# Kernel optimization log

Hardware: AMD Instinct MI355X
Metric: run time of the kernel (lower is better)

## Reference

```python
import jax, jax.numpy as jnp
import numpy as np

H = 4  # pairwise_num_attention_heads

def _layer_norm(x, gamma, beta, eps=1e-5):
    mu = jnp.mean(x, axis=-1, keepdims=True)
    var = jnp.var(x, axis=-1, keepdims=True)
    return (x - mu) * jax.lax.rsqrt(var + eps) * gamma + beta

def setup_inputs() -> dict:
    key = jax.random.key(0)
    ks = jax.random.split(key, 8)
    B, L, P = 1, 256, 128
    s = 0.02
    return {
        "pairwise_states": jax.random.normal(ks[0], (B, L, L, P), jnp.float32),
        "ln_gamma": jnp.ones((P,), jnp.float32),
        "ln_beta": jnp.zeros((P,), jnp.float32),
        "Wq": jax.random.normal(ks[1], (P, P), jnp.float32) * s,
        "Wk": jax.random.normal(ks[2], (P, P), jnp.float32) * s,
        "Wv": jax.random.normal(ks[3], (P, P), jnp.float32) * s,
        "Wb": jax.random.normal(ks[4], (P, H), jnp.float32) * s,
        "Wg": jax.random.normal(ks[5], (P, P), jnp.float32) * s,
        "bg": jnp.zeros((P,), jnp.float32),
        "Wo": jax.random.normal(ks[6], (P, P), jnp.float32) * s,
        "bo": jnp.zeros((P,), jnp.float32),
    }

def reference(pairwise_states, ln_gamma, ln_beta, Wq, Wk, Wv, Wb, Wg, bg, Wo, bo):
    # Row-axis triangle attention (RibonanzaNetPairwiseAttention, axis='row', eval mode).
    B, L, _, P = pairwise_states.shape
    D = P // H  # attention_head_size
    x = _layer_norm(pairwise_states, ln_gamma, ln_beta)  # [b,i,j,p]
    q = (x @ Wq).reshape(B, L, L, H, D)
    k = (x @ Wk).reshape(B, L, L, H, D)
    v = (x @ Wv).reshape(B, L, L, H, D)
    scale = jnp.asarray(D, x.dtype) ** 0.5
    # pairwise bias: [b,i,j,h] -> broadcast over the row axis of the scores
    bias = jnp.einsum('bijp,ph->bhij', x, Wb)  # [b,h,L,L]
    # scores[b,h,i,j,k]: within row i, query position j attends to key position k
    scores = jnp.einsum('bijhd,bikhd->bhijk', q, k) / scale + bias[:, :, None]
    probs = jax.nn.softmax(scores, axis=-1)
    ctx = jnp.einsum('bhijk,bikhd->bijhd', probs, v).reshape(B, L, L, P)
    gate = jax.nn.sigmoid(x @ Wg + bg)
    ctx = gate * ctx
    # output dense + residual (AxisDropout is identity in eval mode)
    return ctx @ Wo + bo + pairwise_states
```

## Files before the change

### kernel.cpp

```cpp
#include <hip/hip_runtime.h>

#define NPOS 65536

typedef __attribute__((ext_vector_type(8))) short bf16x8;
typedef __attribute__((ext_vector_type(4))) float f32x4;

#if __has_builtin(__builtin_amdgcn_exp2f)
#define EXP2F(x) __builtin_amdgcn_exp2f(x)
#else
#define EXP2F(x) __expf((x) * 0.6931471805599453f)
#endif
#if __has_builtin(__builtin_amdgcn_rcpf)
#define RCPF(x) __builtin_amdgcn_rcpf(x)
#else
#define RCPF(x) (1.0f / (x))
#endif

static __device__ __forceinline__ unsigned short f2bf(float f) {
  union { float f; unsigned int u; } v; v.f = f;
  unsigned int r = v.u + 0x7fffu + ((v.u >> 16) & 1u);
  return (unsigned short)(r >> 16);
}
static __device__ __forceinline__ float lo_bf(unsigned int u) {
  union { unsigned int u; float f; } v; v.u = u << 16; return v.f;
}
static __device__ __forceinline__ float hi_bf(unsigned int u) {
  union { unsigned int u; float f; } v; v.u = u & 0xffff0000u; return v.f;
}
static __device__ __forceinline__ unsigned int permpack(float hi, float lo) {
  union { float f; unsigned int u; } a, b;
  a.f = hi; b.f = lo;
#if __has_builtin(__builtin_amdgcn_perm)
  return __builtin_amdgcn_perm(a.u, b.u, 0x07060302u);
#else
  return (a.u & 0xffff0000u) | (b.u >> 16);
#endif
}

__global__ void k_pack(const float* __restrict__ Wq, const float* __restrict__ Wk,
                       const float* __restrict__ Wv, const float* __restrict__ Wg,
                       const float* __restrict__ Wo,
                       ushort* __restrict__ WT, ushort* __restrict__ WoT) {
  int idx = blockIdx.x * blockDim.x + threadIdx.x;
  if (idx < 512 * 128) {
    int n = idx >> 7, k = idx & 127;
    int nn = n & 127;
    float val;
    if (n < 128)      val = Wq[k * 128 + nn] * (0.17677669529663687f * 1.4426950408889634f);
    else if (n < 256) val = Wk[k * 128 + nn];
    else if (n < 384) val = Wv[k * 128 + nn];
    else              val = Wg[k * 128 + nn];
    WT[idx] = f2bf(val);
  } else if (idx < 512 * 128 + 128 * 128) {
    int j = idx - 512 * 128;
    int n = j >> 7, k = j & 127;
    WoT[j] = f2bf(Wo[k * 128 + n]);
  }
}

__global__ __launch_bounds__(128, 4) void k_lnbias(
    const float* __restrict__ in, const float* __restrict__ gamma,
    const float* __restrict__ beta, const float* __restrict__ Wb,
    ushort* __restrict__ biasB) {
  int t = threadIdx.x, wv = t >> 6, lane = t & 63;
  int n = lane & 15, g = lane >> 4;
  int myrow = blockIdx.x * 32 + wv * 16 + n;
  const float* rp = in + (size_t)myrow * 128;

  float xv[32];
  float sm = 0.f, ssm = 0.f;
  #pragma unroll
  for (int kc = 0; kc < 4; kc++)
    #pragma unroll
    for (int pr = 0; pr < 2; pr++) {
      float4 v = *(const float4*)(rp + kc * 32 + g * 8 + pr * 4);
      int o = kc * 8 + pr * 4;
      xv[o] = v.x; xv[o+1] = v.y; xv[o+2] = v.z; xv[o+3] = v.w;
      sm  += v.x + v.y + v.z + v.w;
      ssm += v.x*v.x + v.y*v.y + v.z*v.z + v.w*v.w;
    }
  sm  += __shfl_xor(sm, 16, 64);  sm  += __shfl_xor(sm, 32, 64);
  ssm += __shfl_xor(ssm, 16, 64); ssm += __shfl_xor(ssm, 32, 64);
  float mu  = sm * (1.0f / 128.0f);
  float var = ssm * (1.0f / 128.0f) - mu * mu;
  float rs  = rsqrtf(var + 1e-5f);
  float p0 = 0.f, p1 = 0.f, p2 = 0.f, p3 = 0.f;
  #pragma unroll
  for (int kc = 0; kc < 4; kc++)
    #pragma unroll
    for (int pr = 0; pr < 2; pr++) {
      int c0 = kc * 32 + g * 8 + pr * 4;
      float4 g4 = *(const float4*)(gamma + c0);
      float4 b4 = *(const float4*)(beta + c0);
      int o = kc * 8 + pr * 4;
      #pragma unroll
      for (int r = 0; r < 4; r++) {
        float xn = (xv[o + r] - mu) * rs * (&g4.x)[r] + (&b4.x)[r];
        float4 w = ((const float4*)Wb)[c0 + r];
        p0 += xn * w.x; p1 += xn * w.y; p2 += xn * w.z; p3 += xn * w.w;
      }
    }
  p0 += __shfl_xor(p0, 16, 64); p0 += __shfl_xor(p0, 32, 64);
  p1 += __shfl_xor(p1, 16, 64); p1 += __shfl_xor(p1, 32, 64);
  p2 += __shfl_xor(p2, 16, 64); p2 += __shfl_xor(p2, 32, 64);
  p3 += __shfl_xor(p3, 16, 64); p3 += __shfl_xor(p3, 32, 64);
  if (g == 0) {
    const float l2e = 1.4426950408889634f;
    biasB[0 * NPOS + myrow] = f2bf(p0 * l2e);
    biasB[1 * NPOS + myrow] = f2bf(p1 * l2e);
    biasB[2 * NPOS + myrow] = f2bf(p2 * l2e);
    biasB[3 * NPOS + myrow] = f2bf(p3 * l2e);
  }
}

#define KS 40
#define VS 264
#define QS 40
#define PST 40
__global__ __launch_bounds__(512, 2) void k_attn2(
    const float* __restrict__ in, const float* __restrict__ gamma,
    const float* __restrict__ beta, const ushort* __restrict__ WT,
    const float* __restrict__ bg, const ushort* __restrict__ biasB,
    ushort* __restrict__ gctx) {
  __shared__ __align__(16) ushort Klds[256 * KS];
  __shared__ __align__(16) ushort VTlds[32 * VS];
  __shared__ __align__(16) ushort qstg[8][32 * QS];
  __shared__ __align__(16) ushort pstg[8][16 * PST];
  int i = blockIdx.x >> 2, h = blockIdx.x & 3;
  int t = threadIdx.x, wv = t >> 6, lane = t & 63;
  int n = lane & 15, g = lane >> 4;
  int r0 = wv * 32;

  bf16x8 a[2][4];
  #pragma unroll
  for (int c = 0; c < 2; c++) {
    const float* rp = in + ((size_t)i * 256 + r0 + c * 16 + n) * 128;
    float xv[32];
    float sm = 0.f, ssm = 0.f;
    #pragma unroll
    for (int kc = 0; kc < 4; kc++)
      #pragma unroll
      for (int pr = 0; pr < 2; pr++) {
        float4 v = *(const float4*)(rp + kc * 32 + g * 8 + pr * 4);
        int o = kc * 8 + pr * 4;
        xv[o] = v.x; xv[o+1] = v.y; xv[o+2] = v.z; xv[o+3] = v.w;
        sm  += v.x + v.y + v.z + v.w;
        ssm += v.x*v.x + v.y*v.y + v.z*v.z + v.w*v.w;
      }
    sm  += __shfl_xor(sm, 16, 64);  sm  += __shfl_xor(sm, 32, 64);
    ssm += __shfl_xor(ssm, 16, 64); ssm += __shfl_xor(ssm, 32, 64);
    float mu  = sm * (1.0f / 128.0f);
    float var = ssm * (1.0f / 128.0f) - mu * mu;
    float rs  = rsqrtf(var + 1e-5f);
    #pragma unroll
    for (int kc = 0; kc < 4; kc++)
      #pragma unroll
      for (int pr = 0; pr < 2; pr++) {
        int c0 = kc * 32 + g * 8 + pr * 4;
        float4 g4 = *(const float4*)(gamma + c0);
        float4 b4 = *(const float4*)(beta + c0);
        int o = kc * 8 + pr * 4;
        #pragma unroll
        for (int r = 0; r < 4; r++)
          xv[o + r] = (xv[o + r] - mu) * rs * (&g4.x)[r] + (&b4.x)[r];
      }
    #pragma unroll
    for (int kc = 0; kc < 4; kc++)
      #pragma unroll
      for (int e = 0; e < 8; e++) a[c][kc][e] = (short)f2bf(xv[kc * 8 + e]);
  }

  f32x4 gs[2][2];
  #pragma unroll
  for (int sect = 0; sect < 4; sect++) {
    bf16x8 b[2][4];
    #pragma unroll
    for (int ntl = 0; ntl < 2; ntl++)
      #pragma unroll
      for (int kc = 0; kc < 4; kc++)
        b[ntl][kc] = *(const bf16x8*)(WT + (size_t)(sect * 128 + h * 32 + ntl * 16 + n) * 128 + kc * 32 + g * 8);
    #pragma unroll
    for (int c = 0; c < 2; c++) {
      f32x4 acc[2];
      #pragma unroll
      for (int ntl = 0; ntl < 2; ntl++) {
        f32x4 cc = {0.f, 0.f, 0.f, 0.f};
        #pragma unroll
        for (int kc = 0; kc < 4; kc++)
          cc = __builtin_amdgcn_mfma_f32_16x16x32_bf16(a[c][kc], b[ntl][kc], cc, 0, 0, 0);
        acc[ntl] = cc;
      }
      if (sect == 0) {
        #pragma unroll
        for (int ntl = 0; ntl < 2; ntl++)
          #pragma unroll
          for (int r = 0; r < 4; r++)
            qstg[wv][(c * 16 + g * 4 + r) * QS + ntl * 16 + n] = f2bf(acc[ntl][r]);
      } else if (sect == 1) {
        #pragma unroll
        for (int ntl = 0; ntl < 2; ntl++)
          #pragma unroll
          for (int r = 0; r < 4; r++)
            Klds[(r0 + c * 16 + g * 4 + r) * KS + ntl * 16 + n] = f2bf(acc[ntl][r]);
      } else if (sect == 2) {
        #pragma unroll
        for (int ntl = 0; ntl < 2; ntl++) {
          uint2 vp;
          vp.x = (unsigned int)f2bf(acc[ntl][0]) | ((unsigned int)f2bf(acc[ntl][1]) << 16);
          vp.y = (unsigned int)f2bf(acc[ntl][2]) | ((unsigned int)f2bf(acc[ntl][3]) << 16);
          *(uint2*)(&VTlds[(ntl * 16 + n) * VS + r0 + c * 16 + g * 4]) = vp;
        }
      } else {
        #pragma unroll
        for (int ntl = 0; ntl < 2; ntl++)
          #pragma unroll
          for (int r = 0; r < 4; r++)
            gs[c][ntl][r] = 1.0f / (1.0f + __expf(-(acc[ntl][r] + bg[h * 32 + ntl * 16 + n])));
      }
    }
  }
  __syncthreads();

  const ushort* bb = biasB + (size_t)h * NPOS;
  ushort* Pw = pstg[wv];
  #pragma unroll
  for (int tt = 0; tt < 2; tt++) {
    int j0 = r0 + tt * 16;
    bf16x8 bq = *(const bf16x8*)(&qstg[wv][(tt * 16 + n) * QS + g * 8]);
    f32x4 s[16];
    #pragma unroll
    for (int kt = 0; kt < 16; kt++) {
      uint2 bv = *(const uint2*)(bb + (size_t)(j0 + n) * 256 + kt * 16 + g * 4);
      bf16x8 ak = *(const bf16x8*)(&Klds[(kt * 16 + n) * KS + g * 8]);
      f32x4 cc;
      cc[0] = lo_bf(bv.x); cc[1] = hi_bf(bv.x);
      cc[2] = lo_bf(bv.y); cc[3] = hi_bf(bv.y);
      s[kt] = __builtin_amdgcn_mfma_f32_16x16x32_bf16(ak, bq, cc, 0, 0, 0);
    }
    f32x4 a4 = {0.f, 0.f, 0.f, 0.f};
    #pragma unroll
    for (int kt = 0; kt < 16; kt++) {
      #pragma unroll
      for (int r = 0; r < 4; r++) s[kt][r] = EXP2F(s[kt][r]);
      a4 += s[kt];
    }
    float smm = (a4[0] + a4[1]) + (a4[2] + a4[3]);
    smm += __shfl_xor(smm, 16, 64);
    smm += __shfl_xor(smm, 32, 64);
    float inv = RCPF(smm);
    f32x4 ctx0 = {0.f, 0.f, 0.f, 0.f}, ctx1 = {0.f, 0.f, 0.f, 0.f};
    #pragma unroll
    for (int c8 = 0; c8 < 8; c8++) {
      #pragma unroll
      for (int t2 = 0; t2 < 2; t2++) {
        int kt = c8 * 2 + t2;
        uint2 pp;
        pp.x = permpack(s[kt][1] * inv, s[kt][0] * inv);
        pp.y = permpack(s[kt][3] * inv, s[kt][2] * inv);
        *(uint2*)(&Pw[n * PST + t2 * 16 + g * 4]) = pp;
      }
      bf16x8 ap = *(const bf16x8*)(&Pw[n * PST + g * 8]);
      bf16x8 v0 = *(const bf16x8*)(&VTlds[(size_t)n * VS + c8 * 32 + g * 8]);
      bf16x8 v1 = *(const bf16x8*)(&VTlds[(size_t)(16 + n) * VS + c8 * 32 + g * 8]);
      ctx0 = __builtin_amdgcn_mfma_f32_16x16x32_bf16(ap, v0, ctx0, 0, 0, 0);
      ctx1 = __builtin_amdgcn_mfma_f32_16x16x32_bf16(ap, v1, ctx1, 0, 0, 0);
    }
    #pragma unroll
    for (int r = 0; r < 4; r++) {
      size_t pos = (size_t)i * 256 + j0 + g * 4 + r;
      gctx[pos * 128 + h * 32 + n]      = f2bf(ctx0[r] * gs[tt][0][r]);
      gctx[pos * 128 + h * 32 + 16 + n] = f2bf(ctx1[r] * gs[tt][1][r]);
    }
  }
}

__global__ __launch_bounds__(128, 4) void k_out(
    const ushort* __restrict__ gctx, const ushort* __restrict__ WoT,
    const float* __restrict__ bo, const float* __restrict__ in0,
    float* __restrict__ out) {
  __shared__ __align__(16) float CT[16 * 132];
  int t = threadIdx.x, wv = t >> 6, lane = t & 63;
  int n = lane & 15, g = lane >> 4;
  int row0 = blockIdx.x * 16;
  bf16x8 a[4];
  #pragma unroll
  for (int kc = 0; kc < 4; kc++)
    a[kc] = *(const bf16x8*)(gctx + (size_t)(row0 + n) * 128 + kc * 32 + g * 8);
  #pragma unroll
  for (int ntl2 = 0; ntl2 < 4; ntl2++) {
    int ntl = wv * 4 + ntl2;
    f32x4 acc = {0.f, 0.f, 0.f, 0.f};
    #pragma unroll
    for (int kc = 0; kc < 4; kc++) {
      bf16x8 b = *(const bf16x8*)(WoT + (size_t)(ntl * 16 + n) * 128 + kc * 32 + g * 8);
      acc = __builtin_amdgcn_mfma_f32_16x16x32_bf16(a[kc], b, acc, 0, 0, 0);
    }
    float bov = bo[ntl * 16 + n];
    #pragma unroll
    for (int r = 0; r < 4; r++)
      CT[(g * 4 + r) * 132 + ntl * 16 + n] = acc[r] + bov;
  }
  __syncthreads();
  #pragma unroll
  for (int it = 0; it < 4; it++) {
    int c = it * 128 + t;
    int row = c >> 5, off = (c & 31) * 4;
    f32x4 v = *(const f32x4*)(&CT[row * 132 + off]);
    size_t o = (size_t)(row0 + row) * 128 + off;
    f32x4 r4 = *(const f32x4*)(in0 + o);
    v[0] += r4[0]; v[1] += r4[1]; v[2] += r4[2]; v[3] += r4[3];
    *(f32x4*)(out + o) = v;
  }
}

extern "C" void kernel_launch(void* const* d_in, const int* in_sizes, int n_in,
                              void* d_out, int out_size, void* d_ws, size_t ws_size,
                              hipStream_t stream) {
  const float* in0   = (const float*)d_in[0];
  const float* gamma = (const float*)d_in[1];
  const float* beta  = (const float*)d_in[2];
  const float* Wq    = (const float*)d_in[3];
  const float* Wk    = (const float*)d_in[4];
  const float* Wv    = (const float*)d_in[5];
  const float* Wb    = (const float*)d_in[6];
  const float* Wg    = (const float*)d_in[7];
  const float* bg    = (const float*)d_in[8];
  const float* Wo    = (const float*)d_in[9];
  const float* bo    = (const float*)d_in[10];
  float* out = (float*)d_out;
  char* ws = (char*)d_ws;

  const size_t MB = 1024 * 1024;
  ushort* gctx  = (ushort*)(ws);
  ushort* biasB = (ushort*)(ws + 16 * MB);
  ushort* WT    = (ushort*)(ws + 17 * MB);
  ushort* WoT   = (ushort*)(ws + 17 * MB + 128 * 1024);

  k_pack  <<<320, 256, 0, stream>>>(Wq, Wk, Wv, Wg, Wo, WT, WoT);
  k_lnbias<<<2048, 128, 0, stream>>>(in0, gamma, beta, Wb, biasB);
  k_attn2 <<<1024, 512, 0, stream>>>(in0, gamma, beta, WT, bg, biasB, gctx);
  k_out   <<<4096, 128, 0, stream>>>(gctx, WoT, bo, in0, out);
}
```

Measured before the change: 220.1 us.

## Materialize bf16 layernorm output once and reuse it across heads in attention

The layernorm+bias kernel now also writes the normalized activations as bf16 into a workspace buffer. The attention kernel loads these directly instead of rereading fp32 input and recomputing layernorm in each of the four head blocks per row. This cuts both the redundant global traffic and the repeated ALU work, at the cost of an extra 16 MB write and read. The block index is also remapped so that blocks with the same head sit next to each other, and the bias loads are hoisted ahead of the MFMA loop to expose memory-level parallelism.

```diff
diff --git a/kernel.cpp b/kernel.cpp
--- a/kernel.cpp
+++ b/kernel.cpp
@@ -20,6 +20,9 @@
   union { float f; unsigned int u; } v; v.f = f;
   unsigned int r = v.u + 0x7fffu + ((v.u >> 16) & 1u);
   return (unsigned short)(r >> 16);
+}
+static __device__ __forceinline__ unsigned int pack2(float a, float b) {
+  return (unsigned int)f2bf(a) | ((unsigned int)f2bf(b) << 16);
 }
 static __device__ __forceinline__ float lo_bf(unsigned int u) {
   union { unsigned int u; float f; } v; v.u = u << 16; return v.f;
@@ -58,10 +61,10 @@
   }
 }
 
-__global__ __launch_bounds__(128, 4) void k_lnbias(
+__global__ __launch_bounds__(128, 4) void k_ln(
     const float* __restrict__ in, const float* __restrict__ gamma,
     const float* __restrict__ beta, const float* __restrict__ Wb,
-    ushort* __restrict__ biasB) {
+    ushort* __restrict__ xln, ushort* __restrict__ biasB) {
   int t = threadIdx.x, wv = t >> 6, lane = t & 63;
   int n = lane & 15, g = lane >> 4;
   int myrow = blockIdx.x * 32 + wv * 16 + n;
@@ -96,9 +99,21 @@
       #pragma unroll
       for (int r = 0; r < 4; r++) {
         float xn = (xv[o + r] - mu) * rs * (&g4.x)[r] + (&b4.x)[r];
+        xv[o + r] = xn;
         float4 w = ((const float4*)Wb)[c0 + r];
         p0 += xn * w.x; p1 += xn * w.y; p2 += xn * w.z; p3 += xn * w.w;
       }
+    }
+  #pragma unroll
+  for (int kc = 0; kc < 4; kc++)
+    #pragma unroll
+    for (int pr = 0; pr < 2; pr++) {
+      int o = kc * 8 + pr * 4;
+      uint2 px;
+      px.x = pack2(xv[o + 1], xv[o]);
+      px.x = (unsigned int)f2bf(xv[o]) | ((unsigned int)f2bf(xv[o + 1]) << 16);
+      px.y = (unsigned int)f2bf(xv[o + 2]) | ((unsigned int)f2bf(xv[o + 3]) << 16);
+      *(uint2*)(xln + (size_t)myrow * 128 + kc * 32 + g * 8 + pr * 4) = px;
     }
   p0 += __shfl_xor(p0, 16, 64); p0 += __shfl_xor(p0, 32, 64);
   p1 += __shfl_xor(p1, 16, 64); p1 += __shfl_xor(p1, 32, 64);
@@ -118,57 +133,25 @@
 #define QS 40
 #define PST 40
 __global__ __launch_bounds__(512, 2) void k_attn2(
-    const float* __restrict__ in, const float* __restrict__ gamma,
-    const float* __restrict__ beta, const ushort* __restrict__ WT,
+    const ushort* __restrict__ xln, const ushort* __restrict__ WT,
     const float* __restrict__ bg, const ushort* __restrict__ biasB,
     ushort* __restrict__ gctx) {
   __shared__ __align__(16) ushort Klds[256 * KS];
   __shared__ __align__(16) ushort VTlds[32 * VS];
   __shared__ __align__(16) ushort qstg[8][32 * QS];
   __shared__ __align__(16) ushort pstg[8][16 * PST];
-  int i = blockIdx.x >> 2, h = blockIdx.x & 3;
+  int i = blockIdx.x & 255, h = blockIdx.x >> 8;
   int t = threadIdx.x, wv = t >> 6, lane = t & 63;
   int n = lane & 15, g = lane >> 4;
   int r0 = wv * 32;
 
   bf16x8 a[2][4];
-  #pragma unroll
-  for (int c = 0; c < 2; c++) {
-    const float* rp = in + ((size_t)i * 256 + r0 + c * 16 + n) * 128;
-    float xv[32];
-    float sm = 0.f, ssm = 0.f;
+  const ushort* xb = xln + ((size_t)i * 256 + r0) * 128;
+  #pragma unroll
+  for (int c = 0; c < 2; c++)
     #pragma unroll
     for (int kc = 0; kc < 4; kc++)
-      #pragma unroll
-      for (int pr = 0; pr < 2; pr++) {
-        float4 v = *(const float4*)(rp + kc * 32 + g * 8 + pr * 4);
-        int o = kc * 8 + pr * 4;
-        xv[o] = v.x; xv[o+1] = v.y; xv[o+2] = v.z; xv[o+3] = v.w;
-        sm  += v.x + v.y + v.z + v.w;
-        ssm += v.x*v.x + v.y*v.y + v.z*v.z + v.w*v.w;
-      }
-    sm  += __shfl_xor(sm, 16, 64);  sm  += __shfl_xor(sm, 32, 64);
-    ssm += __shfl_xor(ssm, 16, 64); ssm += __shfl_xor(ssm, 32, 64);
-    float mu  = sm * (1.0f / 128.0f);
-    float var = ssm * (1.0f / 128.0f) - mu * mu;
-    float rs  = rsqrtf(var + 1e-5f);
-    #pragma unroll
-    for (int kc = 0; kc < 4; kc++)
-      #pragma unroll
-      for (int pr = 0; pr < 2; pr++) {
-        int c0 = kc * 32 + g * 8 + pr * 4;
-        float4 g4 = *(const float4*)(gamma + c0);
-        float4 b4 = *(const float4*)(beta + c0);
-        int o = kc * 8 + pr * 4;
-        #pragma unroll
-        for (int r = 0; r < 4; r++)
-          xv[o + r] = (xv[o + r] - mu) * rs * (&g4.x)[r] + (&b4.x)[r];
-      }
-    #pragma unroll
-    for (int kc = 0; kc < 4; kc++)
-      #pragma unroll
-      for (int e = 0; e < 8; e++) a[c][kc][e] = (short)f2bf(xv[kc * 8 + e]);
-  }
+      a[c][kc] = *(const bf16x8*)(xb + (size_t)(c * 16 + n) * 128 + kc * 32 + g * 8);
 
   f32x4 gs[2][2];
   #pragma unroll
@@ -227,14 +210,17 @@
   for (int tt = 0; tt < 2; tt++) {
     int j0 = r0 + tt * 16;
     bf16x8 bq = *(const bf16x8*)(&qstg[wv][(tt * 16 + n) * QS + g * 8]);
+    uint2 bv[16];
+    #pragma unroll
+    for (int kt = 0; kt < 16; kt++)
+      bv[kt] = *(const uint2*)(bb + (size_t)(j0 + n) * 256 + kt * 16 + g * 4);
     f32x4 s[16];
     #pragma unroll
     for (int kt = 0; kt < 16; kt++) {
-      uint2 bv = *(const uint2*)(bb + (size_t)(j0 + n) * 256 + kt * 16 + g * 4);
       bf16x8 ak = *(const bf16x8*)(&Klds[(kt * 16 + n) * KS + g * 8]);
       f32x4 cc;
-      cc[0] = lo_bf(bv.x); cc[1] = hi_bf(bv.x);
-      cc[2] = lo_bf(bv.y); cc[3] = hi_bf(bv.y);
+      cc[0] = lo_bf(bv[kt].x); cc[1] = hi_bf(bv[kt].x);
+      cc[2] = lo_bf(bv[kt].y); cc[3] = hi_bf(bv[kt].y);
       s[kt] = __builtin_amdgcn_mfma_f32_16x16x32_bf16(ak, bq, cc, 0, 0, 0);
     }
     f32x4 a4 = {0.f, 0.f, 0.f, 0.f};
@@ -332,12 +318,13 @@
 
   const size_t MB = 1024 * 1024;
   ushort* gctx  = (ushort*)(ws);
-  ushort* biasB = (ushort*)(ws + 16 * MB);
-  ushort* WT    = (ushort*)(ws + 17 * MB);
-  ushort* WoT   = (ushort*)(ws + 17 * MB + 128 * 1024);
-
-  k_pack  <<<320, 256, 0, stream>>>(Wq, Wk, Wv, Wg, Wo, WT, WoT);
-  k_lnbias<<<2048, 128, 0, stream>>>(in0, gamma, beta, Wb, biasB);
-  k_attn2 <<<1024, 512, 0, stream>>>(in0, gamma, beta, WT, bg, biasB, gctx);
-  k_out   <<<4096, 128, 0, stream>>>(gctx, WoT, bo, in0, out);
-}
+  ushort* xln   = (ushort*)(ws + 16 * MB);
+  ushort* biasB = (ushort*)(ws + 32 * MB);
+  ushort* WT    = (ushort*)(ws + 33 * MB);
+  ushort* WoT   = (ushort*)(ws + 33 * MB + 128 * 1024);
+
+  k_pack <<<320, 256, 0, stream>>>(Wq, Wk, Wv, Wg, Wo, WT, WoT);
+  k_ln   <<<2048, 128, 0, stream>>>(in0, gamma, beta, Wb, xln, biasB);
+  k_attn2<<<1024, 512, 0, stream>>>(xln, WT, bg, biasB, gctx);
+  k_out  <<<4096, 128, 0, stream>>>(gctx, WoT, bo, in0, out);
+}
```

New measurement: 208.7 us. 1.05x faster.
